# Performance work log

Measured on AMD Instinct MI355X. Metric: run time of the kernel, lower is better.

Reference implementation:

```python
import jax, jax.numpy as jnp
import numpy as np

B = 4           # batchsize == poolsize, pool = arange(B)
N_NODES = 32768
N_EDGES = 262144
CH_V = 16
CH_E = 16
HID = 64
CH_MSG = 2 * CH_V + CH_E  # 48


def setup_inputs() -> dict:
    key = jax.random.key(0)
    ks = jax.random.split(key, 8)
    node_vals = jax.random.normal(ks[0], (B, N_NODES, CH_V), jnp.float32) * 0.01
    edge_vals = jax.random.normal(ks[1], (B, N_EDGES, CH_E), jnp.float32) * 0.1
    conn_a = jax.random.randint(ks[2], (N_EDGES,), 0, N_NODES)
    conn_b = jax.random.randint(ks[3], (N_EDGES,), 0, N_NODES)
    w = lambda k, sh: jax.random.normal(k, sh, jnp.float32) * 0.1
    return {
        "node_vals": node_vals, "edge_vals": edge_vals,
        "conn_a": conn_a, "conn_b": conn_b,
        "Wm1": w(ks[4], (CH_MSG, HID)), "bm1": jnp.zeros((HID,), jnp.float32),
        "Wm2": w(ks[5], (HID, CH_MSG)), "bm2": jnp.zeros((CH_MSG,), jnp.float32),
        "Wu1": w(ks[6], (3 * CH_V, HID)), "bu1": jnp.zeros((HID,), jnp.float32),
        "Wu2": w(ks[7], (HID, CH_V)), "bu2": jnp.zeros((CH_V,), jnp.float32),
    }


def reference(node_vals, edge_vals, conn_a, conn_b,
              Wm1, bm1, Wm2, bm2, Wu1, bu1, Wu2, bu2):
    # NeuralGraph.timestep with node_dropout_p = edge_dropout_p = 0 (masks are identity),
    # use_update=True, average_messages=True, nodes=True, edges=True.
    h_a = node_vals[:, conn_a]                      # [B, E, CH_V] gather at source nodes
    h_b = node_vals[:, conn_b]                      # [B, E, CH_V] gather at target nodes
    h = jnp.concatenate([h_a, h_b, edge_vals], -1)  # [B, E, 48]
    # message MLP (Linear -> tanh -> Linear)
    m = jnp.tanh(h @ Wm1 + bm1) @ Wm2 + bm2         # [B, E, 48]
    m_a = m[..., :CH_V]
    m_b = m[..., CH_V:2 * CH_V]
    m_ab = m[..., 2 * CH_V:]
    # scatter-add aggregation per node (index_add_ along node dim)
    agg_a = jnp.zeros((B, N_NODES, CH_V), m.dtype).at[:, conn_a].add(m_a)
    agg_b = jnp.zeros((B, N_NODES, CH_V), m.dtype).at[:, conn_b].add(m_b)
    # count-based averaging (counts clamped to >= 1, matching the buffer fixup)
    ones = jnp.ones((N_EDGES,), m.dtype)
    cnt_a = jnp.maximum(jax.ops.segment_sum(ones, conn_a, num_segments=N_NODES), 1.0)
    cnt_b = jnp.maximum(jax.ops.segment_sum(ones, conn_b, num_segments=N_NODES), 1.0)
    agg_a = agg_a / cnt_a[None, :, None]
    agg_b = agg_b / cnt_b[None, :, None]
    # update MLP
    u_in = jnp.concatenate([agg_a, agg_b, node_vals], -1)   # [B, N, 48]
    updates = jnp.tanh(u_in @ Wu1 + bu1) @ Wu2 + bu2        # [B, N, CH_V]
    new_node_vals = node_vals + updates
    new_edge_vals = edge_vals + m_ab
    return new_node_vals, new_edge_vals
```

## Files before the change

### kernel.cpp

```cpp
#include <hip/hip_runtime.h>
#include <hip/hip_bf16.h>
#include <cstdint>
#include <cstddef>

#define B 4
#define NN 32768
#define NE 262144
#define CV 16
#define CE 16
#define HID 64
#define CM 48

using frag  = __attribute__((ext_vector_type(8))) short;
using f32x4 = __attribute__((ext_vector_type(4))) float;

__device__ __forceinline__ float fast_tanh(float x) {
    float e = __expf(2.0f * x);
    return 1.0f - 2.0f / (e + 1.0f);
}

__device__ __forceinline__ unsigned short f2bf(float x) {
    union { float f; unsigned u; } v; v.f = x;
    unsigned r = (v.u + 0x7FFFu + ((v.u >> 16) & 1u)) >> 16;
    return (unsigned short)r;
}

__device__ __forceinline__ float bf2f(unsigned short x) {
    union { unsigned u; float f; } v; v.u = ((unsigned)x) << 16;
    return v.f;
}

__device__ __forceinline__ unsigned pk2bf(float lo, float hi) {
    union { __hip_bfloat162 h; unsigned u; } v;
    v.h = __float22bfloat162_rn(make_float2(lo, hi));
    return v.u;
}

__device__ __forceinline__ unsigned swo(int row, int byte_off) {
    return (unsigned)((row << 7) + (byte_off ^ ((row & 7) << 4)));
}

__device__ __forceinline__ void acc8(float* a, uint4 v) {
    a[0] += bf2f((unsigned short)(v.x & 0xFFFFu));
    a[1] += bf2f((unsigned short)(v.x >> 16));
    a[2] += bf2f((unsigned short)(v.y & 0xFFFFu));
    a[3] += bf2f((unsigned short)(v.y >> 16));
    a[4] += bf2f((unsigned short)(v.z & 0xFFFFu));
    a[5] += bf2f((unsigned short)(v.z >> 16));
    a[6] += bf2f((unsigned short)(v.w & 0xFFFFu));
    a[7] += bf2f((unsigned short)(v.w >> 16));
}

__global__ __launch_bounds__(256) void count_kernel(
    const int* __restrict__ ca, const int* __restrict__ cb,
    int* __restrict__ cnt_a, int* __restrict__ cnt_b,
    int* __restrict__ rank_a, int* __restrict__ rank_b,
    const float* __restrict__ Wm1, const float* __restrict__ bm1,
    const float* __restrict__ Wm2,
    const float* __restrict__ Wu1, const float* __restrict__ bu1,
    const float* __restrict__ Wu2,
    unsigned short* __restrict__ pW1, unsigned short* __restrict__ pW2,
    unsigned short* __restrict__ pWu1, unsigned short* __restrict__ pWu2)
{
    int i = blockIdx.x * 256 + threadIdx.x;
    rank_a[i] = atomicAdd(&cnt_a[ca[i]], 1);
    rank_b[i] = atomicAdd(&cnt_b[cb[i]], 1);

    if (blockIdx.x == 0) {
        for (int x = threadIdx.x; x < 4 * 2 * 64 * 8; x += 256) {
            int j = x & 7, lane = (x >> 3) & 63, ks = (x >> 9) & 1, mt = x >> 10;
            int m = mt * 16 + (lane & 15);
            int k = ks * 32 + (lane >> 4) * 8 + j;
            float w = (k < 48) ? Wm1[k * 64 + m] : (k == 48 ? bm1[m] : 0.0f);
            pW1[x] = f2bf(w);
        }
    } else if (blockIdx.x == 1) {
        for (int x = threadIdx.x; x < 3 * 2 * 64 * 8; x += 256) {
            int j = x & 7, lane = (x >> 3) & 63, ks = (x >> 9) & 1, mt = x >> 10;
            int m = mt * 16 + (lane & 15);
            int k = ks * 32 + (lane >> 4) * 8 + j;
            pW2[x] = f2bf(Wm2[k * 48 + m]);
        }
    } else if (blockIdx.x == 2) {
        for (int x = threadIdx.x; x < 4 * 2 * 64 * 8; x += 256) {
            int j = x & 7, lane = (x >> 3) & 63, ks = (x >> 9) & 1, mt = x >> 10;
            int m = mt * 16 + (lane & 15);
            int k = ks * 32 + (lane >> 4) * 8 + j;
            float w = (k < 48) ? Wu1[k * 64 + m] : (k == 48 ? bu1[m] : 0.0f);
            pWu1[x] = f2bf(w);
        }
    } else if (blockIdx.x == 3) {
        for (int x = threadIdx.x; x < 2 * 64 * 8; x += 256) {
            int j = x & 7, lane = (x >> 3) & 63, ks = x >> 9;
            int m = lane & 15;
            int k = ks * 32 + (lane >> 4) * 8 + j;
            pWu2[x] = f2bf(Wu2[k * 16 + m]);
        }
    }
}

__global__ __launch_bounds__(1024) void scan_kernel(
    const int* __restrict__ cnt_a, int* __restrict__ start_a,
    const int* __restrict__ cnt_b, int* __restrict__ start_b)
{
    const int* cnt = (blockIdx.x == 0) ? cnt_a : cnt_b;
    int* start     = (blockIdx.x == 0) ? start_a : start_b;

    __shared__ int sw[16];
    int t = threadIdx.x;
    int lane = t & 63;
    int wv   = t >> 6;
    int base = t * 32;

    int local[32];
    int sum = 0;
    const int4* p = (const int4*)(cnt + base);
#pragma unroll
    for (int q = 0; q < 8; q++) {
        int4 v = p[q];
        local[q*4+0] = v.x; local[q*4+1] = v.y; local[q*4+2] = v.z; local[q*4+3] = v.w;
        sum += v.x + v.y + v.z + v.w;
    }
    int inc = sum;
#pragma unroll
    for (int off = 1; off < 64; off <<= 1) {
        int u = __shfl_up(inc, off);
        if (lane >= off) inc += u;
    }
    if (lane == 63) sw[wv] = inc;
    __syncthreads();
    if (wv == 0 && lane < 16) {
        int v = sw[lane];
        int i2 = v;
#pragma unroll
        for (int off = 1; off < 16; off <<= 1) {
            int u = __shfl_up(i2, off);
            if (lane >= off) i2 += u;
        }
        sw[lane] = i2 - v;
    }
    __syncthreads();

    int run = sw[wv] + inc - sum;
    int4* ps = (int4*)(start + base);
#pragma unroll
    for (int q = 0; q < 8; q++) {
        int4 o;
        o.x = run; run += local[q*4+0];
        o.y = run; run += local[q*4+1];
        o.z = run; run += local[q*4+2];
        o.w = run; run += local[q*4+3];
        ps[q] = o;
    }
}

__global__ __launch_bounds__(256, 5) void edge_kernel(
    const float* __restrict__ node_vals, const float* __restrict__ edge_vals,
    const int* __restrict__ ca, const int* __restrict__ cb,
    const int* __restrict__ rank_a, const int* __restrict__ rank_b,
    const int* __restrict__ start_a, const int* __restrict__ start_b,
    const unsigned short* __restrict__ pW1, const unsigned short* __restrict__ pW2,
    const float* __restrict__ bm2,
    float* __restrict__ out_edge,
    unsigned short* __restrict__ ma_csr, unsigned short* __restrict__ mb_csr)
{
    __shared__ unsigned short sH[256 * 64];
    char* sB = (char*)sH;

    int t    = threadIdx.x;
    int lane = t & 63;
    int col  = lane & 15;
    int quad = lane >> 4;
    int erow = (t >> 6) * 64;
    int cha  = quad * 4;

    int bid  = blockIdx.x;
    int xcd  = bid & 7;
    int bb   = xcd >> 1;
    int tile = ((bid >> 3) << 1) | (xcd & 1);
    size_t eb = ((size_t)bb << 18) + ((size_t)tile << 8);

    int posx, posy;
    {
        int e  = (tile << 8) + t;
        size_t idx = eb + t;
        int na = ca[e], nb = cb[e];
        posx = start_a[na] + rank_a[e];
        posy = start_b[nb] + rank_b[e];
        float h[48];
        const float4* pA = (const float4*)(node_vals + ((size_t)bb * NN + na) * CV);
        const float4* pB = (const float4*)(node_vals + ((size_t)bb * NN + nb) * CV);
        const float4* pE = (const float4*)(edge_vals + idx * CE);
#pragma unroll
        for (int q = 0; q < 4; q++) {
            float4 va = pA[q];
            h[q*4+0] = va.x; h[q*4+1] = va.y; h[q*4+2] = va.z; h[q*4+3] = va.w;
            float4 vb = pB[q];
            h[16+q*4+0] = vb.x; h[16+q*4+1] = vb.y; h[16+q*4+2] = vb.z; h[16+q*4+3] = vb.w;
            float4 ve = pE[q];
            h[32+q*4+0] = ve.x; h[32+q*4+1] = ve.y; h[32+q*4+2] = ve.z; h[32+q*4+3] = ve.w;
        }
        unsigned pk[32];
#pragma unroll
        for (int q = 0; q < 24; q++) pk[q] = pk2bf(h[2*q], h[2*q+1]);
        pk[24] = 0x3F80u;
#pragma unroll
        for (int q = 25; q < 32; q++) pk[q] = 0;
        const uint4* src = (const uint4*)pk;
#pragma unroll
        for (int q = 0; q < 8; q++)
            *(uint4*)(sB + swo(t, q * 16)) = src[q];
    }
    asm volatile("s_waitcnt lgkmcnt(0)" ::: "memory");

#pragma unroll
    for (int hh = 0; hh < 2; hh++) {
        int r0 = erow + hh * 32 + col;

        frag w1f[4][2];
#pragma unroll
        for (int mt = 0; mt < 4; mt++)
#pragma unroll
            for (int ks = 0; ks < 2; ks++)
                w1f[mt][ks] = *(const frag*)&pW1[(((mt * 2 + ks) * 64) + lane) * 8];

        f32x4 acc1[4][2];
#pragma unroll
        for (int mt = 0; mt < 4; mt++)
#pragma unroll
            for (int n = 0; n < 2; n++) acc1[mt][n] = (f32x4){0.f, 0.f, 0.f, 0.f};

#pragma unroll
        for (int ks = 0; ks < 2; ks++) {
            frag bfr[2];
#pragma unroll
            for (int n = 0; n < 2; n++)
                bfr[n] = *(const frag*)(sB + swo(r0 + n * 16, ks * 64 + quad * 16));
#pragma unroll
            for (int mt = 0; mt < 4; mt++)
#pragma unroll
                for (int n = 0; n < 2; n++)
                    acc1[mt][n] = __builtin_amdgcn_mfma_f32_16x16x32_bf16(
                        w1f[mt][ks], bfr[n], acc1[mt][n], 0, 0, 0);
        }

#pragma unroll
        for (int n = 0; n < 2; n++) {
            int row = r0 + n * 16;
#pragma unroll
            for (int mt = 0; mt < 4; mt++) {
                uint2 w;
                w.x = pk2bf(fast_tanh(acc1[mt][n][0]), fast_tanh(acc1[mt][n][1]));
                w.y = pk2bf(fast_tanh(acc1[mt][n][2]), fast_tanh(acc1[mt][n][3]));
                *(uint2*)(sB + swo(row, mt * 32 + quad * 8)) = w;
            }
        }
        asm volatile("s_waitcnt lgkmcnt(0)" ::: "memory");

        frag w2f[3][2];
#pragma unroll
        for (int mt = 0; mt < 3; mt++)
#pragma unroll
            for (int ks = 0; ks < 2; ks++)
                w2f[mt][ks] = *(const frag*)&pW2[(((mt * 2 + ks) * 64) + lane) * 8];

        f32x4 acc2[3][2];
#pragma unroll
        for (int mt = 0; mt < 3; mt++)
#pragma unroll
            for (int n = 0; n < 2; n++) acc2[mt][n] = (f32x4){0.f, 0.f, 0.f, 0.f};

#pragma unroll
        for (int ks = 0; ks < 2; ks++) {
            frag bfr[2];
#pragma unroll
            for (int n = 0; n < 2; n++)
                bfr[n] = *(const frag*)(sB + swo(r0 + n * 16, ks * 64 + quad * 16));
#pragma unroll
            for (int mt = 0; mt < 3; mt++)
#pragma unroll
                for (int n = 0; n < 2; n++)
                    acc2[mt][n] = __builtin_amdgcn_mfma_f32_16x16x32_bf16(
                        w2f[mt][ks], bfr[n], acc2[mt][n], 0, 0, 0);
        }

        float4 b2e = *(const float4*)&bm2[32 + cha];
#pragma unroll
        for (int n = 0; n < 2; n++) {
            int le = r0 + n * 16;
            size_t o = (eb + le) * CE + cha;
            float4 ev = *(const float4*)&edge_vals[o];
            float4 ov;
            ov.x = ev.x + acc2[2][n][0] + b2e.x;
            ov.y = ev.y + acc2[2][n][1] + b2e.y;
            ov.z = ev.z + acc2[2][n][2] + b2e.z;
            ov.w = ev.w + acc2[2][n][3] + b2e.w;
            *(float4*)&out_edge[o] = ov;
        }

        float4 b2a = *(const float4*)&bm2[cha];
        float4 b2b = *(const float4*)&bm2[16 + cha];
#pragma unroll
        for (int n = 0; n < 2; n++) {
            int row = r0 + n * 16;
            uint2 wa;
            wa.x = pk2bf(acc2[0][n][0] + b2a.x, acc2[0][n][1] + b2a.y);
            wa.y = pk2bf(acc2[0][n][2] + b2a.z, acc2[0][n][3] + b2a.w);
            *(uint2*)(sB + swo(row, quad * 8)) = wa;
            uint2 wb;
            wb.x = pk2bf(acc2[1][n][0] + b2b.x, acc2[1][n][1] + b2b.y);
            wb.y = pk2bf(acc2[1][n][2] + b2b.z, acc2[1][n][3] + b2b.w);
            *(uint2*)(sB + swo(row, 32 + quad * 8)) = wb;
        }
    }
    asm volatile("s_waitcnt lgkmcnt(0)" ::: "memory");

    {
        uint4 a0 = *(const uint4*)(sB + swo(t, 0));
        uint4 a1 = *(const uint4*)(sB + swo(t, 16));
        uint4 b0 = *(const uint4*)(sB + swo(t, 32));
        uint4 b1 = *(const uint4*)(sB + swo(t, 48));
        unsigned short* pa = &ma_csr[((size_t)bb * NE + posx) * 16];
        *(uint4*)(pa + 0) = a0;
        *(uint4*)(pa + 8) = a1;
        unsigned short* pb = &mb_csr[((size_t)bb * NE + posy) * 16];
        *(uint4*)(pb + 0) = b0;
        *(uint4*)(pb + 8) = b1;
    }
}

__global__ __launch_bounds__(256) void node_kernel(
    const float* __restrict__ node_vals,
    const unsigned short* __restrict__ ma_csr, const unsigned short* __restrict__ mb_csr,
    const int* __restrict__ start_a, const int* __restrict__ start_b,
    const int* __restrict__ cnt_a, const int* __restrict__ cnt_b,
    const unsigned short* __restrict__ pWu1, const unsigned short* __restrict__ pWu2,
    const float* __restrict__ bu2,
    float* __restrict__ out_node)
{
    __shared__ unsigned short sH[256 * 64];
    char* sB = (char*)sH;

    int t    = threadIdx.x;
    int lane = t & 63;
    int col  = lane & 15;
    int quad = lane >> 4;
    int erow = (t >> 6) * 64;
    int cha  = quad * 4;

    int g = blockIdx.x * 256 + t;
    int n = g & (NN - 1);
    int b = g >> 15;

    {
        float ua[16] = {0.f,0.f,0.f,0.f,0.f,0.f,0.f,0.f,0.f,0.f,0.f,0.f,0.f,0.f,0.f,0.f};
        float ub[16] = {0.f,0.f,0.f,0.f,0.f,0.f,0.f,0.f,0.f,0.f,0.f,0.f,0.f,0.f,0.f,0.f};
        int da = cnt_a[n], sa = start_a[n];
        int db = cnt_b[n], sbn = start_b[n];
        const unsigned short* pa = ma_csr + ((size_t)b * NE + sa) * 16;
        const unsigned short* pb = mb_csr + ((size_t)b * NE + sbn) * 16;
        for (int k = 0; k < da; k++) {
            acc8(&ua[0], *(const uint4*)(pa + (size_t)k * 16));
            acc8(&ua[8], *(const uint4*)(pa + (size_t)k * 16 + 8));
        }
        for (int k = 0; k < db; k++) {
            acc8(&ub[0], *(const uint4*)(pb + (size_t)k * 16));
            acc8(&ub[8], *(const uint4*)(pb + (size_t)k * 16 + 8));
        }
        float inva = 1.0f / (float)max(da, 1);
        float invb = 1.0f / (float)max(db, 1);

        float h[48];
        const float4* pn = (const float4*)(node_vals + (size_t)g * CV);
#pragma unroll
        for (int q = 0; q < 16; q++) h[q]      = ua[q] * inva;
#pragma unroll
        for (int q = 0; q < 16; q++) h[16 + q] = ub[q] * invb;
#pragma unroll
        for (int q = 0; q < 4; q++) {
            float4 vn = pn[q];
            h[32+q*4+0] = vn.x; h[32+q*4+1] = vn.y; h[32+q*4+2] = vn.z; h[32+q*4+3] = vn.w;
        }
        unsigned pk[32];
#pragma unroll
        for (int q = 0; q < 24; q++) pk[q] = pk2bf(h[2*q], h[2*q+1]);
        pk[24] = 0x3F80u;
#pragma unroll
        for (int q = 25; q < 32; q++) pk[q] = 0;
        const uint4* src = (const uint4*)pk;
#pragma unroll
        for (int q = 0; q < 8; q++)
            *(uint4*)(sB + swo(t, q * 16)) = src[q];
    }
    asm volatile("s_waitcnt lgkmcnt(0)" ::: "memory");

    frag w1f[4][2];
#pragma unroll
    for (int mt = 0; mt < 4; mt++)
#pragma unroll
        for (int ks = 0; ks < 2; ks++)
            w1f[mt][ks] = *(const frag*)&pWu1[(((mt * 2 + ks) * 64) + lane) * 8];

    f32x4 acc1[4][4];
#pragma unroll
    for (int mt = 0; mt < 4; mt++)
#pragma unroll
        for (int nt = 0; nt < 4; nt++) acc1[mt][nt] = (f32x4){0.f, 0.f, 0.f, 0.f};

#pragma unroll
    for (int ks = 0; ks < 2; ks++) {
        frag bfr[4];
#pragma unroll
        for (int nt = 0; nt < 4; nt++)
            bfr[nt] = *(const frag*)(sB + swo(erow + nt*16 + col, ks * 64 + quad * 16));
#pragma unroll
        for (int mt = 0; mt < 4; mt++)
#pragma unroll
            for (int nt = 0; nt < 4; nt++)
                acc1[mt][nt] = __builtin_amdgcn_mfma_f32_16x16x32_bf16(
                    w1f[mt][ks], bfr[nt], acc1[mt][nt], 0, 0, 0);
    }

#pragma unroll
    for (int nt = 0; nt < 4; nt++) {
        int row = erow + nt*16 + col;
#pragma unroll
        for (int mt = 0; mt < 4; mt++) {
            uint2 w;
            w.x = pk2bf(fast_tanh(acc1[mt][nt][0]), fast_tanh(acc1[mt][nt][1]));
            w.y = pk2bf(fast_tanh(acc1[mt][nt][2]), fast_tanh(acc1[mt][nt][3]));
            *(uint2*)(sB + swo(row, mt * 32 + quad * 8)) = w;
        }
    }
    asm volatile("s_waitcnt lgkmcnt(0)" ::: "memory");

    frag w2f[2];
#pragma unroll
    for (int ks = 0; ks < 2; ks++)
        w2f[ks] = *(const frag*)&pWu2[(ks * 64 + lane) * 8];

    f32x4 acc2[4];
#pragma unroll
    for (int nt = 0; nt < 4; nt++) acc2[nt] = (f32x4){0.f, 0.f, 0.f, 0.f};

#pragma unroll
    for (int ks = 0; ks < 2; ks++) {
        frag bfr[4];
#pragma unroll
        for (int nt = 0; nt < 4; nt++)
            bfr[nt] = *(const frag*)(sB + swo(erow + nt*16 + col, ks * 64 + quad * 16));
#pragma unroll
        for (int nt = 0; nt < 4; nt++)
            acc2[nt] = __builtin_amdgcn_mfma_f32_16x16x32_bf16(
                w2f[ks], bfr[nt], acc2[nt], 0, 0, 0);
    }

    float4 b2 = *(const float4*)&bu2[cha];
#pragma unroll
    for (int nt = 0; nt < 4; nt++) {
        int le = erow + nt*16 + col;
        size_t o = ((size_t)blockIdx.x * 256 + le) * CV + cha;
        float4 nv = *(const float4*)&node_vals[o];
        float4 ov;
        ov.x = nv.x + acc2[nt][0] + b2.x;
        ov.y = nv.y + acc2[nt][1] + b2.y;
        ov.z = nv.z + acc2[nt][2] + b2.z;
        ov.w = nv.w + acc2[nt][3] + b2.w;
        *(float4*)&out_node[o] = ov;
    }
}

extern "C" void kernel_launch(void* const* d_in, const int* in_sizes, int n_in,
                              void* d_out, int out_size, void* d_ws, size_t ws_size,
                              hipStream_t stream) {
    const float* node_vals = (const float*)d_in[0];
    const float* edge_vals = (const float*)d_in[1];
    const int*   ca        = (const int*)d_in[2];
    const int*   cb        = (const int*)d_in[3];
    const float* Wm1 = (const float*)d_in[4];
    const float* bm1 = (const float*)d_in[5];
    const float* Wm2 = (const float*)d_in[6];
    const float* bm2 = (const float*)d_in[7];
    const float* Wu1 = (const float*)d_in[8];
    const float* bu1 = (const float*)d_in[9];
    const float* Wu2 = (const float*)d_in[10];
    const float* bu2 = (const float*)d_in[11];

    float* out_node = (float*)d_out;
    float* out_edge = out_node + (size_t)B * NN * CV;

    unsigned short* ma_csr = (unsigned short*)d_ws;
    unsigned short* mb_csr = ma_csr + (size_t)B * NE * 16;
    int* cnt_a   = (int*)(mb_csr + (size_t)B * NE * 16);
    int* cnt_b   = cnt_a + NN;
    int* start_a = cnt_b + NN;
    int* start_b = start_a + NN;
    int* rank_a  = start_b + NN;
    int* rank_b  = rank_a + NE;
    unsigned short* pW1  = (unsigned short*)(rank_b + NE);
    unsigned short* pW2  = pW1 + 4096;
    unsigned short* pWu1 = pW2 + 3072;
    unsigned short* pWu2 = pWu1 + 4096;

    hipMemsetAsync(cnt_a, 0, 2 * (size_t)NN * sizeof(int), stream);

    count_kernel<<<NE / 256, 256, 0, stream>>>(
        ca, cb, cnt_a, cnt_b, rank_a, rank_b,
        Wm1, bm1, Wm2, Wu1, bu1, Wu2, pW1, pW2, pWu1, pWu2);
    scan_kernel<<<2, 1024, 0, stream>>>(cnt_a, start_a, cnt_b, start_b);
    edge_kernel<<<(B * NE) / 256, 256, 0, stream>>>(
        node_vals, edge_vals, ca, cb, rank_a, rank_b, start_a, start_b,
        pW1, pW2, bm2, out_edge, ma_csr, mb_csr);
    node_kernel<<<(B * NN) / 256, 256, 0, stream>>>(
        node_vals, ma_csr, mb_csr, start_a, start_b, cnt_a, cnt_b,
        pWu1, pWu2, bu2, out_node);
}
```

Measured before the change: 316.7 us.

## Gather bf16 node copy in edge kernel and coalesce residual outputs via LDS

Adds a bf16 copy of node_vals, written in the count kernel, so the random gathers in the edge kernel fetch 32 bytes per node instead of 64. Edge values are loaded once per thread and kept in registers for the residual, and the MFMA outputs are staged through LDS so each thread writes a contiguous 64-byte row for out_edge and out_node. The XCD-aware block-to-tile remapping is dropped in favour of linear indexing, which may reduce L2 locality on the node gathers. The count kernel takes on extra conversion work, and the LDS staging adds shared-memory traffic.

After: 312.8 us. About the same (-1.2%).

```diff
diff --git a/kernel.cpp b/kernel.cpp
--- a/kernel.cpp
+++ b/kernel.cpp
@@ -59,12 +59,24 @@
     const float* __restrict__ Wm2,
     const float* __restrict__ Wu1, const float* __restrict__ bu1,
     const float* __restrict__ Wu2,
+    const float* __restrict__ node_vals,
     unsigned short* __restrict__ pW1, unsigned short* __restrict__ pW2,
-    unsigned short* __restrict__ pWu1, unsigned short* __restrict__ pWu2)
+    unsigned short* __restrict__ pWu1, unsigned short* __restrict__ pWu2,
+    unsigned short* __restrict__ nv16)
 {
     int i = blockIdx.x * 256 + threadIdx.x;
     rank_a[i] = atomicAdd(&cnt_a[ca[i]], 1);
     rank_b[i] = atomicAdd(&cnt_b[cb[i]], 1);
+
+    {
+        int x0 = i * 8;
+        const float4* src = (const float4*)(node_vals + x0);
+        float4 v0 = src[0], v1 = src[1];
+        uint4 o;
+        o.x = pk2bf(v0.x, v0.y); o.y = pk2bf(v0.z, v0.w);
+        o.z = pk2bf(v1.x, v1.y); o.w = pk2bf(v1.z, v1.w);
+        *(uint4*)(nv16 + x0) = o;
+    }
 
     if (blockIdx.x == 0) {
         for (int x = threadIdx.x; x < 4 * 2 * 64 * 8; x += 256) {
@@ -155,7 +167,7 @@
 }
 
 __global__ __launch_bounds__(256, 5) void edge_kernel(
-    const float* __restrict__ node_vals, const float* __restrict__ edge_vals,
+    const unsigned short* __restrict__ nv16, const float* __restrict__ edge_vals,
     const int* __restrict__ ca, const int* __restrict__ cb,
     const int* __restrict__ rank_a, const int* __restrict__ rank_b,
     const int* __restrict__ start_a, const int* __restrict__ start_b,
@@ -172,37 +184,34 @@
     int col  = lane & 15;
     int quad = lane >> 4;
     int erow = (t >> 6) * 64;
-    int cha  = quad * 4;
-
-    int bid  = blockIdx.x;
-    int xcd  = bid & 7;
-    int bb   = xcd >> 1;
-    int tile = ((bid >> 3) << 1) | (xcd & 1);
-    size_t eb = ((size_t)bb << 18) + ((size_t)tile << 8);
-
-    int posx, posy;
+
+    size_t eb  = (size_t)blockIdx.x * 256;
+    size_t idx = eb + t;
+    int e  = (int)(idx & (NE - 1));
+    int bb = (int)(idx >> 18);
+
+    int na = ca[e], nb = cb[e];
+    int posx = start_a[na] + rank_a[e];
+    int posy = start_b[nb] + rank_b[e];
+
+    float4 ev[4];
     {
-        int e  = (tile << 8) + t;
-        size_t idx = eb + t;
-        int na = ca[e], nb = cb[e];
-        posx = start_a[na] + rank_a[e];
-        posy = start_b[nb] + rank_b[e];
-        float h[48];
-        const float4* pA = (const float4*)(node_vals + ((size_t)bb * NN + na) * CV);
-        const float4* pB = (const float4*)(node_vals + ((size_t)bb * NN + nb) * CV);
+        const uint4* gA = (const uint4*)(nv16 + ((size_t)bb * NN + na) * CV);
+        const uint4* gB = (const uint4*)(nv16 + ((size_t)bb * NN + nb) * CV);
+        uint4 a0 = gA[0], a1 = gA[1];
+        uint4 b0 = gB[0], b1 = gB[1];
         const float4* pE = (const float4*)(edge_vals + idx * CE);
 #pragma unroll
+        for (int q = 0; q < 4; q++) ev[q] = pE[q];
+
+        unsigned pk[32];
+        *(uint4*)&pk[0]  = a0;  *(uint4*)&pk[4]  = a1;
+        *(uint4*)&pk[8]  = b0;  *(uint4*)&pk[12] = b1;
+#pragma unroll
         for (int q = 0; q < 4; q++) {
-            float4 va = pA[q];
-            h[q*4+0] = va.x; h[q*4+1] = va.y; h[q*4+2] = va.z; h[q*4+3] = va.w;
-            float4 vb = pB[q];
-            h[16+q*4+0] = vb.x; h[16+q*4+1] = vb.y; h[16+q*4+2] = vb.z; h[16+q*4+3] = vb.w;
-            float4 ve = pE[q];
-            h[32+q*4+0] = ve.x; h[32+q*4+1] = ve.y; h[32+q*4+2] = ve.z; h[32+q*4+3] = ve.w;
-        }
-        unsigned pk[32];
-#pragma unroll
-        for (int q = 0; q < 24; q++) pk[q] = pk2bf(h[2*q], h[2*q+1]);
+            pk[16 + 2*q + 0] = pk2bf(ev[q].x, ev[q].y);
+            pk[16 + 2*q + 1] = pk2bf(ev[q].z, ev[q].w);
+        }
         pk[24] = 0x3F80u;
 #pragma unroll
         for (int q = 25; q < 32; q++) pk[q] = 0;
@@ -284,22 +293,17 @@
                         w2f[mt][ks], bfr[n], acc2[mt][n], 0, 0, 0);
         }
 
-        float4 b2e = *(const float4*)&bm2[32 + cha];
 #pragma unroll
         for (int n = 0; n < 2; n++) {
-            int le = r0 + n * 16;
-            size_t o = (eb + le) * CE + cha;
-            float4 ev = *(const float4*)&edge_vals[o];
-            float4 ov;
-            ov.x = ev.x + acc2[2][n][0] + b2e.x;
-            ov.y = ev.y + acc2[2][n][1] + b2e.y;
-            ov.z = ev.z + acc2[2][n][2] + b2e.z;
-            ov.w = ev.w + acc2[2][n][3] + b2e.w;
-            *(float4*)&out_edge[o] = ov;
-        }
-
-        float4 b2a = *(const float4*)&bm2[cha];
-        float4 b2b = *(const float4*)&bm2[16 + cha];
+            int row = r0 + n * 16;
+            float4 v;
+            v.x = acc2[2][n][0]; v.y = acc2[2][n][1];
+            v.z = acc2[2][n][2]; v.w = acc2[2][n][3];
+            *(float4*)(sB + swo(row, 64 + quad * 16)) = v;
+        }
+
+        float4 b2a = *(const float4*)&bm2[quad * 4];
+        float4 b2b = *(const float4*)&bm2[16 + quad * 4];
 #pragma unroll
         for (int n = 0; n < 2; n++) {
             int row = r0 + n * 16;
@@ -326,6 +330,20 @@
         unsigned short* pb = &mb_csr[((size_t)bb * NE + posy) * 16];
         *(uint4*)(pb + 0) = b0;
         *(uint4*)(pb + 8) = b1;
+
+        const float4* pb2 = (const float4*)&bm2[32];
+        float4* po = (float4*)&out_edge[idx * CE];
+#pragma unroll
+        for (int q = 0; q < 4; q++) {
+            float4 m = *(const float4*)(sB + swo(t, 64 + q * 16));
+            float4 c = pb2[q];
+            float4 o;
+            o.x = ev[q].x + m.x + c.x;
+            o.y = ev[q].y + m.y + c.y;
+            o.z = ev[q].z + m.z + c.z;
+            o.w = ev[q].w + m.w + c.w;
+            po[q] = o;
+        }
     }
 }
 
@@ -346,12 +364,12 @@
     int col  = lane & 15;
     int quad = lane >> 4;
     int erow = (t >> 6) * 64;
-    int cha  = quad * 4;
 
     int g = blockIdx.x * 256 + t;
     int n = g & (NN - 1);
     int b = g >> 15;
 
+    float4 pn[4];
     {
         float ua[16] = {0.f,0.f,0.f,0.f,0.f,0.f,0.f,0.f,0.f,0.f,0.f,0.f,0.f,0.f,0.f,0.f};
         float ub[16] = {0.f,0.f,0.f,0.f,0.f,0.f,0.f,0.f,0.f,0.f,0.f,0.f,0.f,0.f,0.f,0.f};
@@ -370,20 +388,22 @@
         float inva = 1.0f / (float)max(da, 1);
         float invb = 1.0f / (float)max(db, 1);
 
-        float h[48];
-        const float4* pn = (const float4*)(node_vals + (size_t)g * CV);
-#pragma unroll
-        for (int q = 0; q < 16; q++) h[q]      = ua[q] * inva;
-#pragma unroll
-        for (int q = 0; q < 16; q++) h[16 + q] = ub[q] * invb;
+        const float4* pnv = (const float4*)(node_vals + (size_t)g * CV);
+#pragma unroll
+        for (int q = 0; q < 4; q++) pn[q] = pnv[q];
+
+        unsigned pk[32];
+#pragma unroll
+        for (int q = 0; q < 8; q++)
+            pk[q] = pk2bf(ua[2*q] * inva, ua[2*q+1] * inva);
+#pragma unroll
+        for (int q = 0; q < 8; q++)
+            pk[8 + q] = pk2bf(ub[2*q] * invb, ub[2*q+1] * invb);
 #pragma unroll
         for (int q = 0; q < 4; q++) {
-            float4 vn = pn[q];
-            h[32+q*4+0] = vn.x; h[32+q*4+1] = vn.y; h[32+q*4+2] = vn.z; h[32+q*4+3] = vn.w;
-        }
-        unsigned pk[32];
-#pragma unroll
-        for (int q = 0; q < 24; q++) pk[q] = pk2bf(h[2*q], h[2*q+1]);
+            pk[16 + 2*q + 0] = pk2bf(pn[q].x, pn[q].y);
+            pk[16 + 2*q + 1] = pk2bf(pn[q].z, pn[q].w);
+        }
         pk[24] = 0x3F80u;
 #pragma unroll
         for (int q = 25; q < 32; q++) pk[q] = 0;
@@ -455,18 +475,30 @@
                 w2f[ks], bfr[nt], acc2[nt], 0, 0, 0);
     }
 
-    float4 b2 = *(const float4*)&bu2[cha];
 #pragma unroll
     for (int nt = 0; nt < 4; nt++) {
-        int le = erow + nt*16 + col;
-        size_t o = ((size_t)blockIdx.x * 256 + le) * CV + cha;
-        float4 nv = *(const float4*)&node_vals[o];
-        float4 ov;
-        ov.x = nv.x + acc2[nt][0] + b2.x;
-        ov.y = nv.y + acc2[nt][1] + b2.y;
-        ov.z = nv.z + acc2[nt][2] + b2.z;
-        ov.w = nv.w + acc2[nt][3] + b2.w;
-        *(float4*)&out_node[o] = ov;
+        int row = erow + nt*16 + col;
+        float4 v;
+        v.x = acc2[nt][0]; v.y = acc2[nt][1];
+        v.z = acc2[nt][2]; v.w = acc2[nt][3];
+        *(float4*)(sB + swo(row, quad * 16)) = v;
+    }
+    asm volatile("s_waitcnt lgkmcnt(0)" ::: "memory");
+
+    {
+        const float4* pb2 = (const float4*)bu2;
+        float4* po = (float4*)&out_node[(size_t)g * CV];
+#pragma unroll
+        for (int q = 0; q < 4; q++) {
+            float4 m = *(const float4*)(sB + swo(t, q * 16));
+            float4 c = pb2[q];
+            float4 o;
+            o.x = pn[q].x + m.x + c.x;
+            o.y = pn[q].y + m.y + c.y;
+            o.z = pn[q].z + m.z + c.z;
+            o.w = pn[q].w + m.w + c.w;
+            po[q] = o;
+        }
     }
 }
 
@@ -501,15 +533,17 @@
     unsigned short* pW2  = pW1 + 4096;
     unsigned short* pWu1 = pW2 + 3072;
     unsigned short* pWu2 = pWu1 + 4096;
+    unsigned short* nv16 = pWu2 + 1024;
 
     hipMemsetAsync(cnt_a, 0, 2 * (size_t)NN * sizeof(int), stream);
 
     count_kernel<<<NE / 256, 256, 0, stream>>>(
         ca, cb, cnt_a, cnt_b, rank_a, rank_b,
-        Wm1, bm1, Wm2, Wu1, bu1, Wu2, pW1, pW2, pWu1, pWu2);
+        Wm1, bm1, Wm2, Wu1, bu1, Wu2, node_vals,
+        pW1, pW2, pWu1, pWu2, nv16);
     scan_kernel<<<2, 1024, 0, stream>>>(cnt_a, start_a, cnt_b, start_b);
     edge_kernel<<<(B * NE) / 256, 256, 0, stream>>>(
-        node_vals, edge_vals, ca, cb, rank_a, rank_b, start_a, start_b,
+        nv16, edge_vals, ca, cb, rank_a, rank_b, start_a, start_b,
         pW1, pW2, bm2, out_edge, ma_csr, mb_csr);
     node_kernel<<<(B * NN) / 256, 256, 0, stream>>>(
         node_vals, ma_csr, mb_csr, start_a, start_b, cnt_a, cnt_b,
```
